# Kernel tuning notes

Hardware: AMD Instinct MI355X
Metric: run time of the kernel (lower is better)

The kernel has to match this reference:

```python
import jax, jax.numpy as jnp
import numpy as np
import math

K_NEIGH = 8
STRIDE = 4
EPS = 1e-8

def _gather(feats, idx):
    # feats (B,N,D), idx (B,M,K) -> (B,M,K,D)
    return jax.vmap(lambda f, i: f[i])(feats, idx)

def _knn_idx(q, p, k):
    # squared-distance KNN, indices sorted by ascending distance
    d2 = (q * q).sum(-1)[:, :, None] + (p * p).sum(-1)[:, None, :] - 2.0 * jnp.einsum('bmd,bnd->bmn', q, p)
    _, idx = jax.lax.top_k(-d2, k)
    return idx

def _fps(pos, k):
    # farthest point sampling, start at index 0 (pytorch3d default)
    B, N, _ = pos.shape
    start = jnp.zeros((B,), dtype=jnp.int32)
    mind = jnp.full((B, N), jnp.inf, dtype=pos.dtype)
    def body(carry, _):
        mind, last = carry
        lp = jax.vmap(lambda p, i: p[i])(pos, last)  # (B,3)
        d = ((pos - lp[:, None, :]) ** 2).sum(-1)
        mind = jnp.minimum(mind, d)
        nxt = jnp.argmax(mind, axis=-1).astype(jnp.int32)
        return (mind, nxt), nxt
    _, nxts = jax.lax.scan(body, (mind, start), None, length=k - 1)
    idx = jnp.concatenate([start[None], nxts], axis=0).swapaxes(0, 1)  # (B,k)
    fp = jax.vmap(lambda p, i: p[i])(pos, idx)
    return fp

def _gelu(t):
    return jax.nn.gelu(t, approximate=False)

def setup_inputs() -> dict:
    key = jax.random.key(0)
    N, B, D = 8192, 2, 128
    ks = jax.random.split(key, 16)
    w = lambda k, i, o: 0.02 * jax.random.normal(k, (i, o), dtype=jnp.float32)
    return {
        'x': jax.random.normal(ks[0], (N, B, D), dtype=jnp.float32),
        'p_pos': jax.random.uniform(ks[1], (B, N, 3), dtype=jnp.float32),
        'Wq': w(ks[2], D, D), 'bq': jnp.zeros((D,), jnp.float32),
        'Wk': w(ks[3], D, D), 'bk': jnp.zeros((D,), jnp.float32),
        'Wv': w(ks[4], D, D), 'bv': jnp.zeros((D,), jnp.float32),
        'Wpe1': w(ks[5], 3, D), 'bpe1': jnp.zeros((D,), jnp.float32),
        'Wpe2': w(ks[6], D, D), 'bpe2': jnp.zeros((D,), jnp.float32),
        'Wg': w(ks[7], D, D), 'bg': jnp.zeros((D,), jnp.float32),
        'Wo': w(ks[8], D, D), 'bo': jnp.zeros((D,), jnp.float32),
        'scale': jnp.ones((D,), jnp.float32),
        'Wf1': w(ks[9], D, 4 * D), 'bf1': jnp.zeros((4 * D,), jnp.float32),
        'Wf2': w(ks[10], 4 * D, 2 * D), 'bf2': jnp.zeros((2 * D,), jnp.float32),
        'Wpool': w(ks[11], 3 + 2 * D, 2 * D),
    }

def reference(x, p_pos, Wq, bq, Wk, bk, Wv, bv, Wpe1, bpe1, Wpe2, bpe2, Wg, bg, Wo, bo, scale, Wf1, bf1, Wf2, bf2, Wpool):
    D = x.shape[-1]
    # --- PointAttention ---
    xt = jnp.swapaxes(x, 0, 1)                      # (B,N,D)
    q = xt @ Wq + bq
    k = xt @ Wk + bk
    v = xt @ Wv + bv
    idx = _knn_idx(p_pos, p_pos, K_NEIGH)           # (B,N,K)
    knn_pos = _gather(p_pos, idx)                   # (B,N,K,3)
    k_knn = _gather(k, idx)
    v_knn = _gather(v, idx)
    pe = _gelu((p_pos[:, :, None, :] - knn_pos) @ Wpe1 + bpe1) @ Wpe2 + bpe2
    attn = (q[:, :, None, :] - k_knn + pe) @ Wg + bg
    attn = jax.nn.softmax(attn / math.sqrt(D), axis=-1)  # softmax over feature dim, as in source
    res = jnp.einsum('bmnf,bmnf->bmf', attn, v_knn + pe)
    res = res @ Wo + bo
    x = x + jnp.swapaxes(res, 0, 1)                 # (N,B,D)
    # --- RMSNorm ---
    rms = jnp.sqrt((x * x).sum(-1, keepdims=True)) / math.sqrt(D)
    x = scale * (x / (rms + EPS))
    # --- FFN ---
    x = _gelu(x @ Wf1 + bf1) @ Wf2 + bf2            # (N,B,2D)
    # --- PointPool ---
    xt2 = jnp.swapaxes(x, 0, 1)                     # (B,N,2D)
    n_out = p_pos.shape[1] // STRIDE
    fp_pos = jax.lax.stop_gradient(_fps(p_pos, n_out))    # (B,n_out,3)
    kidx = jax.lax.stop_gradient(_knn_idx(fp_pos, p_pos, K_NEIGH))
    knn_x = _gather(xt2, kidx)                      # (B,n_out,K,2D)
    h = jnp.concatenate([jnp.broadcast_to(fp_pos[:, :, None, :], knn_x.shape[:3] + (3,)), knn_x], axis=-1)
    h = h @ Wpool
    h = jnp.where(h >= 0, h, 0.01 * h)              # LeakyReLU(0.01)
    h = h.max(axis=-2)                              # (B,n_out,2D)
    return jnp.swapaxes(h, 0, 1), fp_pos
```

## Files before the change

### kernel.cpp

```cpp
#include <hip/hip_runtime.h>
#include <math.h>

#define N_PTS   8192
#define BATCH   2
#define DIM     128
#define NOUT    2048
#define FPOFF   1048576
#define SLICE_MAX 512

__device__ __forceinline__ float gelu_f(float v) {
  return 0.5f * v * (1.0f + erff(v * 0.70710678118654752440f));
}

__device__ __forceinline__ void knn_insert(float (&dist)[8], int (&idq)[8],
                                           float d2, int ci) {
  if (d2 < dist[7]) {
    float dd = d2;
#pragma unroll
    for (int j = 0; j < 8; ++j) {
      bool cc = dd < dist[j];
      float td = dist[j]; int ti = idq[j];
      dist[j] = cc ? dd : td; idq[j] = cc ? ci : ti;
      dd = cc ? td : dd; ci = cc ? ti : ci;
    }
  }
}

__device__ __forceinline__ void fps_slice(
    const float* __restrict__ P, float* __restrict__ MWS, float* __restrict__ LPWS,
    float* __restrict__ FPWS, float* __restrict__ OUTFP,
    int b, int t0, int t1)
{
  __builtin_amdgcn_s_setprio(3);
  __shared__ unsigned long long wkeys[2][4];
  __shared__ float hist[SLICE_MAX * 3];
  const int tid = threadIdx.x;
  const int wv = tid >> 6;
  const float* __restrict__ Pb = P + (long)b * N_PTS * 3;
  float px[32], py[32], pz[32], mind[32];
#pragma unroll
  for (int s = 0; s < 32; ++s) {
    int i = s * 256 + tid;
    px[s] = Pb[i * 3 + 0];
    py[s] = Pb[i * 3 + 1];
    pz[s] = Pb[i * 3 + 2];
  }
  float lx, ly, lz;
  if (t0 == 0) {
#pragma unroll
    for (int s = 0; s < 32; ++s) mind[s] = INFINITY;
    lx = Pb[0]; ly = Pb[1]; lz = Pb[2];
    if (tid == 0) { hist[0] = lx; hist[1] = ly; hist[2] = lz; }
  } else {
#pragma unroll
    for (int s = 0; s < 32; ++s) mind[s] = MWS[b * N_PTS + s * 256 + tid];
    lx = LPWS[b * 4 + 0]; ly = LPWS[b * 4 + 1]; lz = LPWS[b * 4 + 2];
  }
  const int tstart = (t0 == 0) ? 1 : t0;
  for (int t = tstart; t < t1; ++t) {
    const int par = t & 1;
    float bv = -INFINITY; int bs = 0;
#pragma unroll
    for (int s = 0; s < 32; ++s) {
      float dx = __fsub_rn(px[s], lx);
      float dy = __fsub_rn(py[s], ly);
      float dz = __fsub_rn(pz[s], lz);
      float d = __fadd_rn(__fadd_rn(__fmul_rn(dx, dx), __fmul_rn(dy, dy)), __fmul_rn(dz, dz));
      float mm = fminf(mind[s], d);
      mind[s] = mm;
      bool c = mm > bv;
      bv = c ? mm : bv; bs = c ? s : bs;
    }
    unsigned long long key =
        ((unsigned long long)__float_as_uint(bv) << 32) |
        (unsigned int)~(unsigned int)(bs * 256 + tid);
#pragma unroll
    for (int off = 1; off <= 32; off <<= 1) {
      unsigned long long o = __shfl_xor(key, off);
      key = (o > key) ? o : key;
    }
    if ((tid & 63) == 0) wkeys[par][wv] = key;
    __syncthreads();
    unsigned long long wk = wkeys[par][0];
#pragma unroll
    for (int u = 1; u < 4; ++u) {
      unsigned long long o = wkeys[par][u];
      wk = (o > wk) ? o : wk;
    }
    const int idx = (int)(~(unsigned int)wk);
    lx = Pb[idx * 3 + 0];
    ly = Pb[idx * 3 + 1];
    lz = Pb[idx * 3 + 2];
    if (tid == 0) {
      int h = (t - t0) * 3;
      hist[h + 0] = lx; hist[h + 1] = ly; hist[h + 2] = lz;
    }
  }
#pragma unroll
  for (int s = 0; s < 32; ++s) MWS[b * N_PTS + s * 256 + tid] = mind[s];
  if (tid == 0) { LPWS[b * 4 + 0] = lx; LPWS[b * 4 + 1] = ly; LPWS[b * 4 + 2] = lz; }
  __syncthreads();
  const int cnt = (t1 - t0) * 3;
  const long base = ((long)b * NOUT + t0) * 3;
  for (int i = tid; i < cnt; i += 256) {
    float v2 = hist[i];
    FPWS[base + i] = v2;
    OUTFP[FPOFF + base + i] = v2;
  }
  __builtin_amdgcn_s_setprio(0);
}

__global__ __launch_bounds__(256) void fps_fin(
    const float* __restrict__ P, float* __restrict__ MWS, float* __restrict__ LPWS,
    float* __restrict__ FPWS, float* __restrict__ OUTFP, int t0, int t1)
{
  fps_slice(P, MWS, LPWS, FPWS, OUTFP, blockIdx.x, t0, t1);
}

__global__ __launch_bounds__(256) void gemm_k(
    const float* __restrict__ A, const float* __restrict__ W,
    const float* __restrict__ bias, float* __restrict__ OUT,
    const float* __restrict__ resid,
    int nbx, int nby, int N, int K, int a_mode, int o_mode, int act,
    const float* __restrict__ P, float* __restrict__ MWS, float* __restrict__ LPWS,
    float* __restrict__ FPWS, float* __restrict__ OUTFP, int t0, int t1)
{
  if ((int)blockIdx.x < 2) {
    fps_slice(P, MWS, LPWS, FPWS, OUTFP, (int)blockIdx.x, t0, t1);
    return;
  }
  const int wid = (int)blockIdx.x - 2;
  __shared__ float As[16][132];
  __shared__ float Ws[16][132];
  const int tid = threadIdx.x;
  const int tx = tid & 15, ty = tid >> 4;
  const int bx = wid % nbx;
  const int by = wid / nbx;
  float acc[8][8];
#pragma unroll
  for (int i = 0; i < 8; ++i)
#pragma unroll
    for (int j = 0; j < 8; ++j) acc[i][j] = 0.f;

  for (int k0 = 0; k0 < K; k0 += 16) {
#pragma unroll
    for (int rep = 0; rep < 2; ++rep) {
      int qq = tid + rep * 256;
      int m = qq >> 2, kq = qq & 3;
      int r = by * 128 + m;
      int arow = (a_mode == 1) ? ((r & 8191) * 2 + (r >> 13)) : r;
      const float4 av = *(const float4*)(A + (long)arow * K + k0 + kq * 4);
      As[kq * 4 + 0][m] = av.x; As[kq * 4 + 1][m] = av.y;
      As[kq * 4 + 2][m] = av.z; As[kq * 4 + 3][m] = av.w;
      int kw = qq >> 5, nq = qq & 31;
      const float4 wv = *(const float4*)(W + (long)(k0 + kw) * N + bx * 128 + nq * 4);
      *(float4*)&Ws[kw][nq * 4] = wv;
    }
    __syncthreads();
#pragma unroll
    for (int kk = 0; kk < 16; ++kk) {
      float4 a0 = *(const float4*)&As[kk][ty * 8];
      float4 a1 = *(const float4*)&As[kk][ty * 8 + 4];
      float4 w0 = *(const float4*)&Ws[kk][tx * 4];
      float4 w1 = *(const float4*)&Ws[kk][64 + tx * 4];
      float am[8] = {a0.x, a0.y, a0.z, a0.w, a1.x, a1.y, a1.z, a1.w};
      float wn[8] = {w0.x, w0.y, w0.z, w0.w, w1.x, w1.y, w1.z, w1.w};
#pragma unroll
      for (int i = 0; i < 8; ++i)
#pragma unroll
        for (int j = 0; j < 8; ++j) acc[i][j] += am[i] * wn[j];
    }
    __syncthreads();
  }
  const int c0 = bx * 128 + tx * 4;
  const int c1 = c0 + 64;
  float4 ba = *(const float4*)(bias + c0);
  float4 bb = *(const float4*)(bias + c1);
#pragma unroll
  for (int i = 0; i < 8; ++i) {
    int r = by * 128 + ty * 8 + i;
    int orow = (o_mode == 1) ? ((r & 8191) * 2 + (r >> 13))
             : (o_mode == 2) ? ((r & 1) * 8192 + (r >> 1)) : r;
    float o[8] = {acc[i][0] + ba.x, acc[i][1] + ba.y, acc[i][2] + ba.z, acc[i][3] + ba.w,
                  acc[i][4] + bb.x, acc[i][5] + bb.y, acc[i][6] + bb.z, acc[i][7] + bb.w};
    if (act == 1) {
#pragma unroll
      for (int j = 0; j < 8; ++j) o[j] = gelu_f(o[j]);
    }
    if (resid) {
      float4 r0 = *(const float4*)(resid + (long)orow * N + c0);
      float4 r1 = *(const float4*)(resid + (long)orow * N + c1);
      o[0] += r0.x; o[1] += r0.y; o[2] += r0.z; o[3] += r0.w;
      o[4] += r1.x; o[5] += r1.y; o[6] += r1.z; o[7] += r1.w;
    }
    *(float4*)(OUT + (long)orow * N + c0) = make_float4(o[0], o[1], o[2], o[3]);
    *(float4*)(OUT + (long)orow * N + c1) = make_float4(o[4], o[5], o[6], o[7]);
  }
}

__global__ __launch_bounds__(256) void knn1_k(
    const float* __restrict__ Q, const float* __restrict__ Pp,
    int* __restrict__ OUTI,
    const float* __restrict__ P, float* __restrict__ MWS, float* __restrict__ LPWS,
    float* __restrict__ FPWS, float* __restrict__ OUTFP, int t0, int t1)
{
  if ((int)blockIdx.x < 2) {
    fps_slice(P, MWS, LPWS, FPWS, OUTFP, (int)blockIdx.x, t0, t1);
    return;
  }
  const int wid = (int)blockIdx.x - 2;
  __shared__ float4 shp[512];
  const int b = wid >> 5;
  const int m = (wid & 31) * 256 + threadIdx.x;
  const float qx = Q[(b * N_PTS + m) * 3 + 0];
  const float qy = Q[(b * N_PTS + m) * 3 + 1];
  const float qz = Q[(b * N_PTS + m) * 3 + 2];
  const float sqq = __fadd_rn(__fadd_rn(__fmul_rn(qx, qx), __fmul_rn(qy, qy)), __fmul_rn(qz, qz));
  float dist[8]; int idq[8];
#pragma unroll
  for (int j = 0; j < 8; ++j) { dist[j] = INFINITY; idq[j] = 0; }
  for (int tt = 0; tt < N_PTS; tt += 512) {
    __syncthreads();
    for (int l = threadIdx.x; l < 512; l += 256) {
      float x = Pp[(b * N_PTS + tt + l) * 3 + 0];
      float y = Pp[(b * N_PTS + tt + l) * 3 + 1];
      float z = Pp[(b * N_PTS + tt + l) * 3 + 2];
      float s = __fadd_rn(__fadd_rn(__fmul_rn(x, x), __fmul_rn(y, y)), __fmul_rn(z, z));
      shp[l] = make_float4(x, y, z, s);
    }
    __syncthreads();
    for (int c = 0; c < 512; c += 4) {
      float4 p0 = shp[c + 0];
      float4 p1 = shp[c + 1];
      float4 p2 = shp[c + 2];
      float4 p3 = shp[c + 3];
      float d0 = __fsub_rn(__fadd_rn(sqq, p0.w), __fmul_rn(2.0f,
                 __fadd_rn(__fadd_rn(__fmul_rn(qx, p0.x), __fmul_rn(qy, p0.y)), __fmul_rn(qz, p0.z))));
      float d1 = __fsub_rn(__fadd_rn(sqq, p1.w), __fmul_rn(2.0f,
                 __fadd_rn(__fadd_rn(__fmul_rn(qx, p1.x), __fmul_rn(qy, p1.y)), __fmul_rn(qz, p1.z))));
      float d2 = __fsub_rn(__fadd_rn(sqq, p2.w), __fmul_rn(2.0f,
                 __fadd_rn(__fadd_rn(__fmul_rn(qx, p2.x), __fmul_rn(qy, p2.y)), __fmul_rn(qz, p2.z))));
      float d3 = __fsub_rn(__fadd_rn(sqq, p3.w), __fmul_rn(2.0f,
                 __fadd_rn(__fadd_rn(__fmul_rn(qx, p3.x), __fmul_rn(qy, p3.y)), __fmul_rn(qz, p3.z))));
      float mn = fminf(fminf(d0, d1), fminf(d2, d3));
      if (mn < dist[7]) {
        knn_insert(dist, idq, d0, tt + c + 0);
        knn_insert(dist, idq, d1, tt + c + 1);
        knn_insert(dist, idq, d2, tt + c + 2);
        knn_insert(dist, idq, d3, tt + c + 3);
      }
    }
  }
#pragma unroll
  for (int j = 0; j < 8; ++j) OUTI[(long)(b * N_PTS + m) * 8 + j] = idq[j];
}

__global__ __launch_bounds__(64) void knn2_k(
    const float* __restrict__ Q, const float* __restrict__ P,
    int* __restrict__ OUTI)
{
  __shared__ float4 shp[512];
  const int b = blockIdx.y;
  const int m = blockIdx.x * 64 + threadIdx.x;
  const float qx = Q[(b * NOUT + m) * 3 + 0];
  const float qy = Q[(b * NOUT + m) * 3 + 1];
  const float qz = Q[(b * NOUT + m) * 3 + 2];
  const float sqq = __fadd_rn(__fadd_rn(__fmul_rn(qx, qx), __fmul_rn(qy, qy)), __fmul_rn(qz, qz));
  float dist[8]; int idq[8];
#pragma unroll
  for (int j = 0; j < 8; ++j) { dist[j] = INFINITY; idq[j] = 0; }
  for (int tt = 0; tt < N_PTS; tt += 512) {
    __syncthreads();
    for (int l = threadIdx.x; l < 512; l += 64) {
      float x = P[(b * N_PTS + tt + l) * 3 + 0];
      float y = P[(b * N_PTS + tt + l) * 3 + 1];
      float z = P[(b * N_PTS + tt + l) * 3 + 2];
      float s = __fadd_rn(__fadd_rn(__fmul_rn(x, x), __fmul_rn(y, y)), __fmul_rn(z, z));
      shp[l] = make_float4(x, y, z, s);
    }
    __syncthreads();
    for (int c = 0; c < 512; c += 4) {
      float4 p0 = shp[c + 0];
      float4 p1 = shp[c + 1];
      float4 p2 = shp[c + 2];
      float4 p3 = shp[c + 3];
      float d0 = __fsub_rn(__fadd_rn(sqq, p0.w), __fmul_rn(2.0f,
                 __fadd_rn(__fadd_rn(__fmul_rn(qx, p0.x), __fmul_rn(qy, p0.y)), __fmul_rn(qz, p0.z))));
      float d1 = __fsub_rn(__fadd_rn(sqq, p1.w), __fmul_rn(2.0f,
                 __fadd_rn(__fadd_rn(__fmul_rn(qx, p1.x), __fmul_rn(qy, p1.y)), __fmul_rn(qz, p1.z))));
      float d2 = __fsub_rn(__fadd_rn(sqq, p2.w), __fmul_rn(2.0f,
                 __fadd_rn(__fadd_rn(__fmul_rn(qx, p2.x), __fmul_rn(qy, p2.y)), __fmul_rn(qz, p2.z))));
      float d3 = __fsub_rn(__fadd_rn(sqq, p3.w), __fmul_rn(2.0f,
                 __fadd_rn(__fadd_rn(__fmul_rn(qx, p3.x), __fmul_rn(qy, p3.y)), __fmul_rn(qz, p3.z))));
      float mn = fminf(fminf(d0, d1), fminf(d2, d3));
      if (mn < dist[7]) {
        knn_insert(dist, idq, d0, tt + c + 0);
        knn_insert(dist, idq, d1, tt + c + 1);
        knn_insert(dist, idq, d2, tt + c + 2);
        knn_insert(dist, idq, d3, tt + c + 3);
      }
    }
  }
#pragma unroll
  for (int j = 0; j < 8; ++j) OUTI[(long)(b * NOUT + m) * 8 + j] = idq[j];
}

__global__ __launch_bounds__(256) void attn_k(
    const float* __restrict__ Qb, const float* __restrict__ Kb, const float* __restrict__ Vb,
    const float* __restrict__ Pp, const int* __restrict__ IDX,
    const float* __restrict__ Wpe1, const float* __restrict__ bpe1,
    const float* __restrict__ Wpe2, const float* __restrict__ bpe2,
    const float* __restrict__ Wg, const float* __restrict__ bg,
    float* __restrict__ RES,
    const float* __restrict__ P, float* __restrict__ MWS, float* __restrict__ LPWS,
    float* __restrict__ FPWS, float* __restrict__ OUTFP, int t0, int t1)
{
  if ((int)blockIdx.x < 2) {
    fps_slice(P, MWS, LPWS, FPWS, OUTFP, (int)blockIdx.x, t0, t1);
    return;
  }
  __shared__ float sbuf[4][1024];
  const int tid = threadIdx.x;
  const int w = tid >> 6, lane = tid & 63;
  const int g = ((int)blockIdx.x - 2) * 4 + w;
  const int b = g >> 13, n = g & 8191;
  const int j0 = lane * 2;
  float* sb = sbuf[w];
  const float2 qv = *(const float2*)(Qb + (long)g * 128 + j0);
  int nb[8];
#pragma unroll
  for (int kk = 0; kk < 8; ++kk) nb[kk] = IDX[g * 8 + kk];
  const float p0 = Pp[(b * N_PTS + n) * 3 + 0];
  const float p1 = Pp[(b * N_PTS + n) * 3 + 1];
  const float p2 = Pp[(b * N_PTS + n) * 3 + 2];
  const float2 w1a = *(const float2*)(Wpe1 + j0);
  const float2 w1b = *(const float2*)(Wpe1 + 128 + j0);
  const float2 w1c = *(const float2*)(Wpe1 + 256 + j0);
  const float2 b1 = *(const float2*)(bpe1 + j0);
#pragma unroll
  for (int kk = 0; kk < 8; ++kk) {
    const float* pn = Pp + (long)(b * N_PTS + nb[kk]) * 3;
    float r0 = p0 - pn[0], r1 = p1 - pn[1], r2 = p2 - pn[2];
    float h0 = r0 * w1a.x + r1 * w1b.x + r2 * w1c.x + b1.x;
    float h1 = r0 * w1a.y + r1 * w1b.y + r2 * w1c.y + b1.y;
    sb[kk * 128 + j0]     = gelu_f(h0);
    sb[kk * 128 + j0 + 1] = gelu_f(h1);
  }
  __syncthreads();
  float2 pe[8];
#pragma unroll
  for (int kk = 0; kk < 8; ++kk) pe[kk] = make_float2(0.f, 0.f);
  for (int i = 0; i < 128; i += 2) {
    float2 wa = *(const float2*)(Wpe2 + (long)i * 128 + j0);
    float2 wb = *(const float2*)(Wpe2 + (long)(i + 1) * 128 + j0);
#pragma unroll
    for (int kk = 0; kk < 8; ++kk) {
      float2 hh = *(const float2*)&sb[kk * 128 + i];
      pe[kk].x += hh.x * wa.x + hh.y * wb.x;
      pe[kk].y += hh.x * wa.y + hh.y * wb.y;
    }
  }
  const float2 b2v = *(const float2*)(bpe2 + j0);
  __syncthreads();
#pragma unroll
  for (int kk = 0; kk < 8; ++kk) {
    pe[kk].x += b2v.x; pe[kk].y += b2v.y;
    const float2 kv = *(const float2*)(Kb + (long)(b * N_PTS + nb[kk]) * 128 + j0);
    sb[kk * 128 + j0]     = qv.x - kv.x + pe[kk].x;
    sb[kk * 128 + j0 + 1] = qv.y - kv.y + pe[kk].y;
  }
  __syncthreads();
  float2 av[8];
#pragma unroll
  for (int kk = 0; kk < 8; ++kk) av[kk] = make_float2(0.f, 0.f);
  for (int i = 0; i < 128; i += 2) {
    float2 wa = *(const float2*)(Wg + (long)i * 128 + j0);
    float2 wb = *(const float2*)(Wg + (long)(i + 1) * 128 + j0);
#pragma unroll
    for (int kk = 0; kk < 8; ++kk) {
      float2 tt = *(const float2*)&sb[kk * 128 + i];
      av[kk].x += tt.x * wa.x + tt.y * wb.x;
      av[kk].y += tt.x * wa.y + tt.y * wb.y;
    }
  }
  const float2 bgv = *(const float2*)(bg + j0);
  float2 resv = make_float2(0.f, 0.f);
  const float sd = 11.313708498984761f;
#pragma unroll
  for (int kk = 0; kk < 8; ++kk) {
    float l0 = (av[kk].x + bgv.x) / sd;
    float l1 = (av[kk].y + bgv.y) / sd;
    float mx = fmaxf(l0, l1);
#pragma unroll
    for (int off = 32; off >= 1; off >>= 1) mx = fmaxf(mx, __shfl_xor(mx, off));
    float e0 = expf(l0 - mx), e1 = expf(l1 - mx);
    float sm = e0 + e1;
#pragma unroll
    for (int off = 32; off >= 1; off >>= 1) sm += __shfl_xor(sm, off);
    const float2 vv = *(const float2*)(Vb + (long)(b * N_PTS + nb[kk]) * 128 + j0);
    resv.x += (e0 / sm) * (vv.x + pe[kk].x);
    resv.y += (e1 / sm) * (vv.y + pe[kk].y);
  }
  *(float2*)(RES + (long)g * 128 + j0) = resv;
}

__global__ __launch_bounds__(256) void rms_k(
    float* __restrict__ X, const float* __restrict__ scale,
    const float* __restrict__ P, float* __restrict__ MWS, float* __restrict__ LPWS,
    float* __restrict__ FPWS, float* __restrict__ OUTFP, int t0, int t1)
{
  if ((int)blockIdx.x < 2) {
    fps_slice(P, MWS, LPWS, FPWS, OUTFP, (int)blockIdx.x, t0, t1);
    return;
  }
  const int tid = threadIdx.x;
  const int w = tid >> 6, lane = tid & 63;
  const long row = (long)((int)blockIdx.x - 2) * 4 + w;
  float2 xv = *(float2*)(X + row * 128 + lane * 2);
  float ss = xv.x * xv.x + xv.y * xv.y;
#pragma unroll
  for (int off = 32; off >= 1; off >>= 1) ss += __shfl_xor(ss, off);
  const float rms = sqrtf(ss) / 11.313708498984761f;
  const float den = rms + 1e-8f;
  const float2 sc = *(const float2*)(scale + lane * 2);
  float2 o;
  o.x = sc.x * (xv.x / den);
  o.y = sc.y * (xv.y / den);
  *(float2*)(X + row * 128 + lane * 2) = o;
}

__global__ __launch_bounds__(256) void pool_k(
    const float* __restrict__ X3, const float* __restrict__ FPWS,
    const int* __restrict__ KIDX, const float* __restrict__ Wp,
    float* __restrict__ OUT)
{
  __shared__ float sh[8][256];
  __shared__ float fp3[3];
  const int bm = blockIdx.x;
  const int b = bm >> 11;
  const int m = bm & 2047;
  const int tid = threadIdx.x;
#pragma unroll
  for (int kk = 0; kk < 8; ++kk) {
    int nbk = KIDX[bm * 8 + kk];
    sh[kk][tid] = X3[(long)(b * N_PTS + nbk) * 256 + tid];
  }
  if (tid < 3) fp3[tid] = FPWS[bm * 3 + tid];
  __syncthreads();
  float base = fp3[0] * Wp[tid] + fp3[1] * Wp[256 + tid] + fp3[2] * Wp[512 + tid];
  float acc[8];
#pragma unroll
  for (int kk = 0; kk < 8; ++kk) acc[kk] = base;
  for (int i = 0; i < 256; i += 2) {
    float w0 = Wp[(3 + i) * 256 + tid];
    float w1 = Wp[(4 + i) * 256 + tid];
#pragma unroll
    for (int kk = 0; kk < 8; ++kk) {
      float2 hh = *(const float2*)&sh[kk][i];
      acc[kk] += hh.x * w0 + hh.y * w1;
    }
  }
  float mx = -INFINITY;
#pragma unroll
  for (int kk = 0; kk < 8; ++kk) {
    float a = acc[kk];
    a = (a >= 0.f) ? a : 0.01f * a;
    mx = fmaxf(mx, a);
  }
  OUT[(long)(m * 2 + b) * 256 + tid] = mx;
}

extern "C" void kernel_launch(void* const* d_in, const int* in_sizes, int n_in,
                              void* d_out, int out_size, void* d_ws, size_t ws_size,
                              hipStream_t stream)
{
  (void)in_sizes; (void)n_in; (void)out_size; (void)ws_size;
  const float* x    = (const float*)d_in[0];
  const float* ppos = (const float*)d_in[1];
  const float* Wq = (const float*)d_in[2];   const float* bq = (const float*)d_in[3];
  const float* Wk = (const float*)d_in[4];   const float* bk = (const float*)d_in[5];
  const float* Wv = (const float*)d_in[6];   const float* bv = (const float*)d_in[7];
  const float* Wpe1 = (const float*)d_in[8]; const float* bpe1 = (const float*)d_in[9];
  const float* Wpe2 = (const float*)d_in[10];const float* bpe2 = (const float*)d_in[11];
  const float* Wg = (const float*)d_in[12];  const float* bg = (const float*)d_in[13];
  const float* Wo = (const float*)d_in[14];  const float* bo = (const float*)d_in[15];
  const float* scale = (const float*)d_in[16];
  const float* Wf1 = (const float*)d_in[17]; const float* bf1 = (const float*)d_in[18];
  const float* Wf2 = (const float*)d_in[19]; const float* bf2 = (const float*)d_in[20];
  const float* Wpool = (const float*)d_in[21];
  float* out = (float*)d_out;
  char* ws = (char*)d_ws;

  float* qb   = (float*)(ws);
  float* kb   = (float*)(ws + (size_t)8 * 1024 * 1024);
  float* vb   = (float*)(ws + (size_t)16 * 1024 * 1024);
  float* res  = (float*)(ws + (size_t)24 * 1024 * 1024);
  float* x2   = (float*)(ws + (size_t)32 * 1024 * 1024);
  float* hbuf = (float*)(ws);
  float* x3   = (float*)(ws + (size_t)32 * 1024 * 1024);
  char*  tail = ws + (size_t)48 * 1024 * 1024;
  int*   idx1 = (int*)  (tail);
  int*   kidx2= (int*)  (tail + 524288);
  float* fpws = (float*)(tail + 655360);
  float* MWS  = (float*)(tail + 720896);
  float* LPWS = (float*)(tail + 786432);

  gemm_k<<<dim3(130), dim3(256), 0, stream>>>(x, Wq, bq, qb, nullptr, 1, 128, 128, 128, 1, 0, 0,
                                              ppos, MWS, LPWS, fpws, out, 0, 140);
  gemm_k<<<dim3(130), dim3(256), 0, stream>>>(x, Wk, bk, kb, nullptr, 1, 128, 128, 128, 1, 0, 0,
                                              ppos, MWS, LPWS, fpws, out, 140, 280);
  gemm_k<<<dim3(130), dim3(256), 0, stream>>>(x, Wv, bv, vb, nullptr, 1, 128, 128, 128, 1, 0, 0,
                                              ppos, MWS, LPWS, fpws, out, 280, 420);
  knn1_k<<<dim3(66), dim3(256), 0, stream>>>(ppos, ppos, idx1,
                                             ppos, MWS, LPWS, fpws, out, 420, 650);
  attn_k<<<dim3(4098), dim3(256), 0, stream>>>(qb, kb, vb, ppos, idx1,
                                               Wpe1, bpe1, Wpe2, bpe2, Wg, bg, res,
                                               ppos, MWS, LPWS, fpws, out, 650, 1150);
  gemm_k<<<dim3(130), dim3(256), 0, stream>>>(res, Wo, bo, x2, x, 1, 128, 128, 128, 0, 1, 0,
                                              ppos, MWS, LPWS, fpws, out, 1150, 1290);
  rms_k<<<dim3(4098), dim3(256), 0, stream>>>(x2, scale,
                                              ppos, MWS, LPWS, fpws, out, 1290, 1350);
  gemm_k<<<dim3(514), dim3(256), 0, stream>>>(x2, Wf1, bf1, hbuf, nullptr, 4, 128, 512, 128, 0, 0, 1,
                                              ppos, MWS, LPWS, fpws, out, 1350, 1630);
  gemm_k<<<dim3(258), dim3(256), 0, stream>>>(hbuf, Wf2, bf2, x3, nullptr, 2, 128, 256, 512, 0, 2, 0,
                                              ppos, MWS, LPWS, fpws, out, 1630, 1910);
  fps_fin<<<dim3(2), dim3(256), 0, stream>>>(ppos, MWS, LPWS, fpws, out, 1910, 2048);
  knn2_k<<<dim3(32, 2), dim3(64), 0, stream>>>(fpws, ppos, kidx2);
  pool_k<<<dim3(4096), dim3(256), 0, stream>>>(x3, fpws, kidx2, Wpool, out);
}
```

Measured before the change: 3.641 ms.

## Widen FPS blocks to 512 threads and rebalance piggybacked FPS slices

The serial farthest-point-sampling slices that ride in blocks 0-1 of each kernel now use 512 threads, so each thread holds 16 points instead of 32, which shortens the per-iteration dependent chain. The GEMM, attention and RMS kernels are widened to 512-thread blocks, with two 256-thread teams per GEMM block, to match. knn1 is split out as a standalone 64-thread-block kernel with no FPS work, and the FPS step ranges are redistributed across the remaining launches. The cost is an extra 8-way wave reduction per FPS step, with more FPS steps left for the final serial fps_fin launch.

New measurement: 3.747 ms. +2.9%, slower.

```diff
diff --git a/kernel.cpp b/kernel.cpp
--- a/kernel.cpp
+++ b/kernel.cpp
@@ -32,15 +32,15 @@
     int b, int t0, int t1)
 {
   __builtin_amdgcn_s_setprio(3);
-  __shared__ unsigned long long wkeys[2][4];
+  __shared__ unsigned long long wkeys[2][8];
   __shared__ float hist[SLICE_MAX * 3];
   const int tid = threadIdx.x;
   const int wv = tid >> 6;
   const float* __restrict__ Pb = P + (long)b * N_PTS * 3;
-  float px[32], py[32], pz[32], mind[32];
-#pragma unroll
-  for (int s = 0; s < 32; ++s) {
-    int i = s * 256 + tid;
+  float px[16], py[16], pz[16], mind[16];
+#pragma unroll
+  for (int s = 0; s < 16; ++s) {
+    int i = s * 512 + tid;
     px[s] = Pb[i * 3 + 0];
     py[s] = Pb[i * 3 + 1];
     pz[s] = Pb[i * 3 + 2];
@@ -48,12 +48,12 @@
   float lx, ly, lz;
   if (t0 == 0) {
 #pragma unroll
-    for (int s = 0; s < 32; ++s) mind[s] = INFINITY;
+    for (int s = 0; s < 16; ++s) mind[s] = INFINITY;
     lx = Pb[0]; ly = Pb[1]; lz = Pb[2];
     if (tid == 0) { hist[0] = lx; hist[1] = ly; hist[2] = lz; }
   } else {
 #pragma unroll
-    for (int s = 0; s < 32; ++s) mind[s] = MWS[b * N_PTS + s * 256 + tid];
+    for (int s = 0; s < 16; ++s) mind[s] = MWS[b * N_PTS + s * 512 + tid];
     lx = LPWS[b * 4 + 0]; ly = LPWS[b * 4 + 1]; lz = LPWS[b * 4 + 2];
   }
   const int tstart = (t0 == 0) ? 1 : t0;
@@ -61,7 +61,7 @@
     const int par = t & 1;
     float bv = -INFINITY; int bs = 0;
 #pragma unroll
-    for (int s = 0; s < 32; ++s) {
+    for (int s = 0; s < 16; ++s) {
       float dx = __fsub_rn(px[s], lx);
       float dy = __fsub_rn(py[s], ly);
       float dz = __fsub_rn(pz[s], lz);
@@ -73,7 +73,7 @@
     }
     unsigned long long key =
         ((unsigned long long)__float_as_uint(bv) << 32) |
-        (unsigned int)~(unsigned int)(bs * 256 + tid);
+        (unsigned int)~(unsigned int)(bs * 512 + tid);
 #pragma unroll
     for (int off = 1; off <= 32; off <<= 1) {
       unsigned long long o = __shfl_xor(key, off);
@@ -83,7 +83,7 @@
     __syncthreads();
     unsigned long long wk = wkeys[par][0];
 #pragma unroll
-    for (int u = 1; u < 4; ++u) {
+    for (int u = 1; u < 8; ++u) {
       unsigned long long o = wkeys[par][u];
       wk = (o > wk) ? o : wk;
     }
@@ -97,12 +97,12 @@
     }
   }
 #pragma unroll
-  for (int s = 0; s < 32; ++s) MWS[b * N_PTS + s * 256 + tid] = mind[s];
+  for (int s = 0; s < 16; ++s) MWS[b * N_PTS + s * 512 + tid] = mind[s];
   if (tid == 0) { LPWS[b * 4 + 0] = lx; LPWS[b * 4 + 1] = ly; LPWS[b * 4 + 2] = lz; }
   __syncthreads();
   const int cnt = (t1 - t0) * 3;
   const long base = ((long)b * NOUT + t0) * 3;
-  for (int i = tid; i < cnt; i += 256) {
+  for (int i = tid; i < cnt; i += 512) {
     float v2 = hist[i];
     FPWS[base + i] = v2;
     OUTFP[FPOFF + base + i] = v2;
@@ -110,18 +110,18 @@
   __builtin_amdgcn_s_setprio(0);
 }
 
-__global__ __launch_bounds__(256) void fps_fin(
+__global__ __launch_bounds__(512) void fps_fin(
     const float* __restrict__ P, float* __restrict__ MWS, float* __restrict__ LPWS,
     float* __restrict__ FPWS, float* __restrict__ OUTFP, int t0, int t1)
 {
   fps_slice(P, MWS, LPWS, FPWS, OUTFP, blockIdx.x, t0, t1);
 }
 
-__global__ __launch_bounds__(256) void gemm_k(
+__global__ __launch_bounds__(512) void gemm2_k(
     const float* __restrict__ A, const float* __restrict__ W,
     const float* __restrict__ bias, float* __restrict__ OUT,
     const float* __restrict__ resid,
-    int nbx, int nby, int N, int K, int a_mode, int o_mode, int act,
+    int nbx, int N, int K, int a_mode, int o_mode, int act,
     const float* __restrict__ P, float* __restrict__ MWS, float* __restrict__ LPWS,
     float* __restrict__ FPWS, float* __restrict__ OUTFP, int t0, int t1)
 {
@@ -130,12 +130,13 @@
     return;
   }
   const int wid = (int)blockIdx.x - 2;
-  __shared__ float As[16][132];
-  __shared__ float Ws[16][132];
-  const int tid = threadIdx.x;
+  __shared__ float As[2][16][132];
+  __shared__ float Ws2[2][16][132];
+  const int team = threadIdx.x >> 8;
+  const int tid = threadIdx.x & 255;
   const int tx = tid & 15, ty = tid >> 4;
   const int bx = wid % nbx;
-  const int by = wid / nbx;
+  const int byy = (wid / nbx) * 2 + team;
   float acc[8][8];
 #pragma unroll
   for (int i = 0; i < 8; ++i)
@@ -147,22 +148,22 @@
     for (int rep = 0; rep < 2; ++rep) {
       int qq = tid + rep * 256;
       int m = qq >> 2, kq = qq & 3;
-      int r = by * 128 + m;
+      int r = byy * 128 + m;
       int arow = (a_mode == 1) ? ((r & 8191) * 2 + (r >> 13)) : r;
       const float4 av = *(const float4*)(A + (long)arow * K + k0 + kq * 4);
-      As[kq * 4 + 0][m] = av.x; As[kq * 4 + 1][m] = av.y;
-      As[kq * 4 + 2][m] = av.z; As[kq * 4 + 3][m] = av.w;
+      As[team][kq * 4 + 0][m] = av.x; As[team][kq * 4 + 1][m] = av.y;
+      As[team][kq * 4 + 2][m] = av.z; As[team][kq * 4 + 3][m] = av.w;
       int kw = qq >> 5, nq = qq & 31;
       const float4 wv = *(const float4*)(W + (long)(k0 + kw) * N + bx * 128 + nq * 4);
-      *(float4*)&Ws[kw][nq * 4] = wv;
+      *(float4*)&Ws2[team][kw][nq * 4] = wv;
     }
     __syncthreads();
 #pragma unroll
     for (int kk = 0; kk < 16; ++kk) {
-      float4 a0 = *(const float4*)&As[kk][ty * 8];
-      float4 a1 = *(const float4*)&As[kk][ty * 8 + 4];
-      float4 w0 = *(const float4*)&Ws[kk][tx * 4];
-      float4 w1 = *(const float4*)&Ws[kk][64 + tx * 4];
+      float4 a0 = *(const float4*)&As[team][kk][ty * 8];
+      float4 a1 = *(const float4*)&As[team][kk][ty * 8 + 4];
+      float4 w0 = *(const float4*)&Ws2[team][kk][tx * 4];
+      float4 w1 = *(const float4*)&Ws2[team][kk][64 + tx * 4];
       float am[8] = {a0.x, a0.y, a0.z, a0.w, a1.x, a1.y, a1.z, a1.w};
       float wn[8] = {w0.x, w0.y, w0.z, w0.w, w1.x, w1.y, w1.z, w1.w};
 #pragma unroll
@@ -178,7 +179,7 @@
   float4 bb = *(const float4*)(bias + c1);
 #pragma unroll
   for (int i = 0; i < 8; ++i) {
-    int r = by * 128 + ty * 8 + i;
+    int r = byy * 128 + ty * 8 + i;
     int orow = (o_mode == 1) ? ((r & 8191) * 2 + (r >> 13))
              : (o_mode == 2) ? ((r & 1) * 8192 + (r >> 1)) : r;
     float o[8] = {acc[i][0] + ba.x, acc[i][1] + ba.y, acc[i][2] + ba.z, acc[i][3] + ba.w,
@@ -198,20 +199,13 @@
   }
 }
 
-__global__ __launch_bounds__(256) void knn1_k(
-    const float* __restrict__ Q, const float* __restrict__ Pp,
-    int* __restrict__ OUTI,
-    const float* __restrict__ P, float* __restrict__ MWS, float* __restrict__ LPWS,
-    float* __restrict__ FPWS, float* __restrict__ OUTFP, int t0, int t1)
-{
-  if ((int)blockIdx.x < 2) {
-    fps_slice(P, MWS, LPWS, FPWS, OUTFP, (int)blockIdx.x, t0, t1);
-    return;
-  }
-  const int wid = (int)blockIdx.x - 2;
+__global__ __launch_bounds__(64) void knn1_k(
+    const float* __restrict__ Q, const float* __restrict__ P,
+    int* __restrict__ OUTI)
+{
   __shared__ float4 shp[512];
-  const int b = wid >> 5;
-  const int m = (wid & 31) * 256 + threadIdx.x;
+  const int b = blockIdx.y;
+  const int m = blockIdx.x * 64 + threadIdx.x;
   const float qx = Q[(b * N_PTS + m) * 3 + 0];
   const float qy = Q[(b * N_PTS + m) * 3 + 1];
   const float qz = Q[(b * N_PTS + m) * 3 + 2];
@@ -221,10 +215,10 @@
   for (int j = 0; j < 8; ++j) { dist[j] = INFINITY; idq[j] = 0; }
   for (int tt = 0; tt < N_PTS; tt += 512) {
     __syncthreads();
-    for (int l = threadIdx.x; l < 512; l += 256) {
-      float x = Pp[(b * N_PTS + tt + l) * 3 + 0];
-      float y = Pp[(b * N_PTS + tt + l) * 3 + 1];
-      float z = Pp[(b * N_PTS + tt + l) * 3 + 2];
+    for (int l = threadIdx.x; l < 512; l += 64) {
+      float x = P[(b * N_PTS + tt + l) * 3 + 0];
+      float y = P[(b * N_PTS + tt + l) * 3 + 1];
+      float z = P[(b * N_PTS + tt + l) * 3 + 2];
       float s = __fadd_rn(__fadd_rn(__fmul_rn(x, x), __fmul_rn(y, y)), __fmul_rn(z, z));
       shp[l] = make_float4(x, y, z, s);
     }
@@ -305,7 +299,7 @@
   for (int j = 0; j < 8; ++j) OUTI[(long)(b * NOUT + m) * 8 + j] = idq[j];
 }
 
-__global__ __launch_bounds__(256) void attn_k(
+__global__ __launch_bounds__(512) void attn_k(
     const float* __restrict__ Qb, const float* __restrict__ Kb, const float* __restrict__ Vb,
     const float* __restrict__ Pp, const int* __restrict__ IDX,
     const float* __restrict__ Wpe1, const float* __restrict__ bpe1,
@@ -319,10 +313,10 @@
     fps_slice(P, MWS, LPWS, FPWS, OUTFP, (int)blockIdx.x, t0, t1);
     return;
   }
-  __shared__ float sbuf[4][1024];
+  __shared__ float sbuf[8][1024];
   const int tid = threadIdx.x;
   const int w = tid >> 6, lane = tid & 63;
-  const int g = ((int)blockIdx.x - 2) * 4 + w;
+  const int g = ((int)blockIdx.x - 2) * 8 + w;
   const int b = g >> 13, n = g & 8191;
   const int j0 = lane * 2;
   float* sb = sbuf[w];
@@ -404,7 +398,7 @@
   *(float2*)(RES + (long)g * 128 + j0) = resv;
 }
 
-__global__ __launch_bounds__(256) void rms_k(
+__global__ __launch_bounds__(512) void rms_k(
     float* __restrict__ X, const float* __restrict__ scale,
     const float* __restrict__ P, float* __restrict__ MWS, float* __restrict__ LPWS,
     float* __restrict__ FPWS, float* __restrict__ OUTFP, int t0, int t1)
@@ -415,7 +409,7 @@
   }
   const int tid = threadIdx.x;
   const int w = tid >> 6, lane = tid & 63;
-  const long row = (long)((int)blockIdx.x - 2) * 4 + w;
+  const long row = (long)((int)blockIdx.x - 2) * 8 + w;
   float2 xv = *(float2*)(X + row * 128 + lane * 2);
   float ss = xv.x * xv.x + xv.y * xv.y;
 #pragma unroll
@@ -505,26 +499,25 @@
   float* MWS  = (float*)(tail + 720896);
   float* LPWS = (float*)(tail + 786432);
 
-  gemm_k<<<dim3(130), dim3(256), 0, stream>>>(x, Wq, bq, qb, nullptr, 1, 128, 128, 128, 1, 0, 0,
-                                              ppos, MWS, LPWS, fpws, out, 0, 140);
-  gemm_k<<<dim3(130), dim3(256), 0, stream>>>(x, Wk, bk, kb, nullptr, 1, 128, 128, 128, 1, 0, 0,
-                                              ppos, MWS, LPWS, fpws, out, 140, 280);
-  gemm_k<<<dim3(130), dim3(256), 0, stream>>>(x, Wv, bv, vb, nullptr, 1, 128, 128, 128, 1, 0, 0,
-                                              ppos, MWS, LPWS, fpws, out, 280, 420);
-  knn1_k<<<dim3(66), dim3(256), 0, stream>>>(ppos, ppos, idx1,
-                                             ppos, MWS, LPWS, fpws, out, 420, 650);
-  attn_k<<<dim3(4098), dim3(256), 0, stream>>>(qb, kb, vb, ppos, idx1,
+  knn1_k<<<dim3(128, 2), dim3(64), 0, stream>>>(ppos, ppos, idx1);
+  gemm2_k<<<dim3(66), dim3(512), 0, stream>>>(x, Wq, bq, qb, nullptr, 1, 128, 128, 1, 0, 0,
+                                              ppos, MWS, LPWS, fpws, out, 0, 160);
+  gemm2_k<<<dim3(66), dim3(512), 0, stream>>>(x, Wk, bk, kb, nullptr, 1, 128, 128, 1, 0, 0,
+                                              ppos, MWS, LPWS, fpws, out, 160, 320);
+  gemm2_k<<<dim3(66), dim3(512), 0, stream>>>(x, Wv, bv, vb, nullptr, 1, 128, 128, 1, 0, 0,
+                                              ppos, MWS, LPWS, fpws, out, 320, 480);
+  attn_k<<<dim3(2050), dim3(512), 0, stream>>>(qb, kb, vb, ppos, idx1,
                                                Wpe1, bpe1, Wpe2, bpe2, Wg, bg, res,
-                                               ppos, MWS, LPWS, fpws, out, 650, 1150);
-  gemm_k<<<dim3(130), dim3(256), 0, stream>>>(res, Wo, bo, x2, x, 1, 128, 128, 128, 0, 1, 0,
-                                              ppos, MWS, LPWS, fpws, out, 1150, 1290);
-  rms_k<<<dim3(4098), dim3(256), 0, stream>>>(x2, scale,
-                                              ppos, MWS, LPWS, fpws, out, 1290, 1350);
-  gemm_k<<<dim3(514), dim3(256), 0, stream>>>(x2, Wf1, bf1, hbuf, nullptr, 4, 128, 512, 128, 0, 0, 1,
-                                              ppos, MWS, LPWS, fpws, out, 1350, 1630);
-  gemm_k<<<dim3(258), dim3(256), 0, stream>>>(hbuf, Wf2, bf2, x3, nullptr, 2, 128, 256, 512, 0, 2, 0,
-                                              ppos, MWS, LPWS, fpws, out, 1630, 1910);
-  fps_fin<<<dim3(2), dim3(256), 0, stream>>>(ppos, MWS, LPWS, fpws, out, 1910, 2048);
+                                               ppos, MWS, LPWS, fpws, out, 480, 900);
+  gemm2_k<<<dim3(66), dim3(512), 0, stream>>>(res, Wo, bo, x2, x, 1, 128, 128, 0, 1, 0,
+                                              ppos, MWS, LPWS, fpws, out, 900, 1060);
+  rms_k<<<dim3(2050), dim3(512), 0, stream>>>(x2, scale,
+                                              ppos, MWS, LPWS, fpws, out, 1060, 1140);
+  gemm2_k<<<dim3(258), dim3(512), 0, stream>>>(x2, Wf1, bf1, hbuf, nullptr, 4, 512, 128, 0, 0, 1,
+                                               ppos, MWS, LPWS, fpws, out, 1140, 1370);
+  gemm2_k<<<dim3(130), dim3(512), 0, stream>>>(hbuf, Wf2, bf2, x3, nullptr, 2, 256, 512, 0, 2, 0,
+                                               ppos, MWS, LPWS, fpws, out, 1370, 1600);
+  fps_fin<<<dim3(2), dim3(512), 0, stream>>>(ppos, MWS, LPWS, fpws, out, 1600, 2048);
   knn2_k<<<dim3(32, 2), dim3(64), 0, stream>>>(fpws, ppos, kidx2);
   pool_k<<<dim3(4096), dim3(256), 0, stream>>>(x3, fpws, kidx2, Wpool, out);
 }
```
